# Performance work log

Hardware: AMD Instinct MI355X
Metric: run time of the kernel (lower is better)

Reference implementation:

```python
import jax, jax.numpy as jnp
import numpy as np

COMMITMENT_COST = 0.25
NUM_EMBEDDINGS = 512
EMBEDDING_DIM = 64


def setup_inputs() -> dict:
    key = jax.random.key(0)
    k1, k2 = jax.random.split(key)
    B, T = 64, 1024
    inputs = jax.random.normal(k1, (B, T, EMBEDDING_DIM), dtype=jnp.float32)
    # matches nn.Embedding init uniform_(-1/K, 1/K)
    embedding = jax.random.uniform(
        k2, (NUM_EMBEDDINGS, EMBEDDING_DIM), dtype=jnp.float32,
        minval=-1.0 / NUM_EMBEDDINGS, maxval=1.0 / NUM_EMBEDDINGS)
    return {"inputs": inputs, "embedding": embedding}


def reference(inputs, embedding):
    B = inputs.shape[0]
    K, D = embedding.shape
    flat = inputs.reshape(-1, D)  # [N, D]
    # squared-euclidean distances [N, K] (same expansion as torch source)
    distances = (
        jnp.sum(flat * flat, axis=1, keepdims=True)
        + jnp.sum(embedding * embedding, axis=1)
        - 2.0 * flat @ embedding.T
    )
    idx = jnp.argmin(distances, axis=1)  # [N]
    # one-hot @ embedding  ==  gather
    quantized = embedding[idx].reshape(inputs.shape)

    e_latent_loss = jnp.mean((jax.lax.stop_gradient(quantized) - inputs) ** 2)
    q_latent_loss = jnp.mean((quantized - jax.lax.stop_gradient(inputs)) ** 2)
    loss = q_latent_loss + COMMITMENT_COST * e_latent_loss

    # straight-through estimator
    quantized_st = inputs + jax.lax.stop_gradient(quantized - inputs)

    # avg_probs = mean of one-hot encodings == histogram of indices / N
    counts = jax.ops.segment_sum(
        jnp.ones(flat.shape[0], dtype=jnp.float32), idx, num_segments=K)
    avg_probs = counts / flat.shape[0]
    perplexity = jnp.exp(-jnp.sum(avg_probs * jnp.log(avg_probs + 1e-10)))

    indices_for_transformer = idx.reshape(B, -1)
    return loss, quantized_st, perplexity, indices_for_transformer
```

## Files before the change

### kernel.cpp

```cpp
#include <hip/hip_runtime.h>
#include <math.h>

#define D 64
#define K 512
#define BLOCK 256
#define ROWS 128
#define KT 128
#define NKT (K / KT)
#define NPART 32


__device__ __forceinline__ float np_sumsq64(const float* v) {
#pragma clang fp contract(off)
    float r[8];
#pragma unroll
    for (int m = 0; m < 8; ++m) r[m] = v[m] * v[m];
#pragma unroll
    for (int i = 8; i < 64; i += 8) {
#pragma unroll
        for (int m = 0; m < 8; ++m) r[m] = r[m] + v[i + m] * v[i + m];
    }
    return ((r[0] + r[1]) + (r[2] + r[3])) + ((r[4] + r[5]) + (r[6] + r[7]));
}

__global__ __launch_bounds__(BLOCK, 2) void vq_fused(
    const float* __restrict__ x, const float* __restrict__ emb,
    float* __restrict__ q_out, float* __restrict__ idx_out,
    float* __restrict__ block_sums, int* __restrict__ part_hist, int N)
{
    __shared__ float4 xs4[ROWS * 16];
    __shared__ float4 es4[KT * 16];
    __shared__ float sx_s[ROWS];
    __shared__ float se_s[KT];
    __shared__ int hist[K];
    __shared__ float red[BLOCK / 64];

    const int tid = threadIdx.x;
    const int rg = tid & 15;
    const int cg = tid >> 4;
    const int rowbase = blockIdx.x * ROWS;

    for (int k2 = tid; k2 < K; k2 += BLOCK) hist[k2] = 0;

    const float4* xsrc = (const float4*)(x + (size_t)rowbase * D);
#pragma unroll
    for (int i = 0; i < (ROWS * 16) / BLOCK; ++i) {
        int f = tid + i * BLOCK;
        int row = f >> 4, jc = f & 15;
        xs4[row * 16 + (jc ^ ((row >> 3) & 7))] = xsrc[f];
    }
    __syncthreads();

    if (tid < ROWS) {
        float xr[D];
        const int sw = (tid >> 3) & 7;
#pragma unroll
        for (int jc = 0; jc < 16; ++jc) {
            float4 v = xs4[tid * 16 + (jc ^ sw)];
            xr[4 * jc + 0] = v.x; xr[4 * jc + 1] = v.y;
            xr[4 * jc + 2] = v.z; xr[4 * jc + 3] = v.w;
        }
        sx_s[tid] = np_sumsq64(xr);
    }

    float bd[8], bkf[8];
#pragma unroll
    for (int r = 0; r < 8; ++r) { bd[r] = INFINITY; bkf[r] = 0.f; }

    const int xbase = rg * 8, ebase = cg * 8;
    const int swx0 = rg & 7, swe0 = cg & 7;

    for (int kt = 0; kt < NKT; ++kt) {
        const float4* esrc = (const float4*)(emb + (size_t)kt * KT * D);
#pragma unroll
        for (int i = 0; i < (KT * 16) / BLOCK; ++i) {
            int f = tid + i * BLOCK;
            int row = f >> 4, jc = f & 15;
            es4[row * 16 + (jc ^ ((row >> 3) & 7))] = esrc[f];
        }
        __syncthreads();

        if (tid < KT) {
            float er[D];
            const int sw = (tid >> 3) & 7;
#pragma unroll
            for (int jc = 0; jc < 16; ++jc) {
                float4 v = es4[tid * 16 + (jc ^ sw)];
                er[4 * jc + 0] = v.x; er[4 * jc + 1] = v.y;
                er[4 * jc + 2] = v.z; er[4 * jc + 3] = v.w;
            }
            se_s[tid] = np_sumsq64(er);
        }

        float acc[8][8];
#pragma unroll
        for (int r = 0; r < 8; ++r)
#pragma unroll
            for (int c = 0; c < 8; ++c) acc[r][c] = 0.f;

#pragma unroll 2
        for (int jc = 0; jc < 16; ++jc) {
            float4 xa[8], eb[8];
#pragma unroll
            for (int r = 0; r < 8; ++r)
                xa[r] = xs4[(xbase + r) * 16 + (jc ^ swx0)];
#pragma unroll
            for (int c = 0; c < 8; ++c)
                eb[c] = es4[(ebase + c) * 16 + (jc ^ swe0)];
#pragma unroll
            for (int r = 0; r < 8; ++r)
#pragma unroll
                for (int c = 0; c < 8; ++c) {
                    acc[r][c] = fmaf(xa[r].x, eb[c].x, acc[r][c]);
                    acc[r][c] = fmaf(xa[r].y, eb[c].y, acc[r][c]);
                    acc[r][c] = fmaf(xa[r].z, eb[c].z, acc[r][c]);
                    acc[r][c] = fmaf(xa[r].w, eb[c].w, acc[r][c]);
                }
        }
        __syncthreads();

        const int kglob = kt * KT + ebase;
        float sev[8];
#pragma unroll
        for (int c = 0; c < 8; ++c) sev[c] = se_s[ebase + c];
#pragma unroll
        for (int r = 0; r < 8; ++r) {
            float sxv = sx_s[xbase + r];
#pragma unroll
            for (int c = 0; c < 8; ++c) {
                float dcur = (sxv + sev[c]) - 2.0f * acc[r][c];
                if (dcur < bd[r]) { bd[r] = dcur; bkf[r] = (float)(kglob + c); }
            }
        }
    }

    __syncthreads();
    float2* bests = (float2*)es4;
#pragma unroll
    for (int r = 0; r < 8; ++r)
        bests[(xbase + r) * 16 + cg] = make_float2(bd[r], bkf[r]);
    __syncthreads();

    float s = 0.f;
    if (tid < ROWS) {
        float bdd = INFINITY, bjf = 1e30f;
#pragma unroll
        for (int g = 0; g < 16; ++g) {
            float2 p = bests[tid * 16 + g];
            if (p.x < bdd || (p.x == bdd && p.y < bjf)) { bdd = p.x; bjf = p.y; }
        }
        const int bi = (int)bjf;
        atomicAdd(&hist[bi], 1);

        const int rowg = rowbase + tid;
        const float4* ep = (const float4*)(emb + (size_t)bi * D);
        float4* qp = (float4*)(q_out + (size_t)rowg * D);
        const int sw = (tid >> 3) & 7;
#pragma unroll
        for (int jc = 0; jc < 16; ++jc) {
            float4 xv = xs4[tid * 16 + (jc ^ sw)];
            float4 e  = ep[jc];
            float dx0 = e.x - xv.x, dx1 = e.y - xv.y;
            float dx2 = e.z - xv.z, dx3 = e.w - xv.w;
            s = fmaf(dx0, dx0, s);
            s = fmaf(dx1, dx1, s);
            s = fmaf(dx2, dx2, s);
            s = fmaf(dx3, dx3, s);
            float4 qs;
            qs.x = xv.x + dx0; qs.y = xv.y + dx1;
            qs.z = xv.z + dx2; qs.w = xv.w + dx3;
            qp[jc] = qs;
        }
        idx_out[rowg] = (float)bi;
    }

    for (int off = 32; off; off >>= 1) s += __shfl_down(s, off, 64);
    if ((tid & 63) == 0) red[tid >> 6] = s;
    __syncthreads();
    if (tid == 0) {
        float t = 0.f;
#pragma unroll
        for (int w = 0; w < BLOCK / 64; ++w) t += red[w];
        block_sums[blockIdx.x] = t;
    }
    const int part = (int)(blockIdx.x & (NPART - 1));
    for (int k2 = tid; k2 < K; k2 += BLOCK) {
        int h = hist[k2];
        if (h) atomicAdd(&part_hist[part * K + k2], h);
    }
}

__global__ __launch_bounds__(512) void vq_finalize(
    const float* __restrict__ block_sums, int nblocks,
    const int* __restrict__ part_hist, float* __restrict__ out_loss,
    float* __restrict__ out_perp, float inv_nelem, float inv_rows)
{
    const int tid = threadIdx.x;
    double ls = 0.0;
    for (int i = tid; i < nblocks; i += 512) ls += (double)block_sums[i];
    int c = 0;
#pragma unroll
    for (int pp = 0; pp < NPART; ++pp) c += part_hist[pp * K + tid];
    double ps = 0.0;
    {
        float p = (float)c * inv_rows;
        ps = (double)(p * logf(p + 1e-10f));
    }
    for (int off = 32; off; off >>= 1) {
        ls += __shfl_down(ls, off, 64);
        ps += __shfl_down(ps, off, 64);
    }
    __shared__ double l8[8], p8[8];
    if ((tid & 63) == 0) { l8[tid >> 6] = ls; p8[tid >> 6] = ps; }
    __syncthreads();
    if (tid == 0) {
        double L = 0.0, P = 0.0;
#pragma unroll
        for (int w = 0; w < 8; ++w) { L += l8[w]; P += p8[w]; }
        *out_loss = 1.25f * (float)(L * (double)inv_nelem);
        *out_perp = expf((float)(-P));
    }
}

extern "C" void kernel_launch(void* const* d_in, const int* in_sizes, int n_in,
                              void* d_out, int out_size, void* d_ws, size_t ws_size,
                              hipStream_t stream) {
    const float* x   = (const float*)d_in[0];
    const float* emb = (const float*)d_in[1];
    const int N = in_sizes[0] / D;
    const int nblocks = N / ROWS;

    float* out      = (float*)d_out;
    float* loss_out = out;
    float* q_out    = out + 1;
    float* perp_out = out + 1 + (size_t)N * D;
    float* idx_out  = perp_out + 1;

    float* block_sums = (float*)d_ws;
    int*   part_hist  = (int*)((char*)d_ws + (((size_t)nblocks * 4 + 255) & ~(size_t)255));

    hipMemsetAsync(part_hist, 0, NPART * K * sizeof(int), stream);
    vq_fused<<<nblocks, BLOCK, 0, stream>>>(x, emb, q_out, idx_out,
                                            block_sums, part_hist, N);
    vq_finalize<<<1, 512, 0, stream>>>(block_sums, nblocks, part_hist,
                                       loss_out, perp_out,
                                       1.0f / (float)((size_t)N * D),
                                       1.0f / (float)N);
}
```

Before: 139.8 us.

## Fuse finalize into main kernel via last-block counter; precompute norms with shuffles

```diff
diff --git a/kernel.cpp b/kernel.cpp
--- a/kernel.cpp
+++ b/kernel.cpp
@@ -10,37 +10,28 @@
 #define NPART 32
 
 
-__device__ __forceinline__ float np_sumsq64(const float* v) {
-#pragma clang fp contract(off)
-    float r[8];
-#pragma unroll
-    for (int m = 0; m < 8; ++m) r[m] = v[m] * v[m];
-#pragma unroll
-    for (int i = 8; i < 64; i += 8) {
-#pragma unroll
-        for (int m = 0; m < 8; ++m) r[m] = r[m] + v[i + m] * v[i + m];
-    }
-    return ((r[0] + r[1]) + (r[2] + r[3])) + ((r[4] + r[5]) + (r[6] + r[7]));
-}
-
 __global__ __launch_bounds__(BLOCK, 2) void vq_fused(
     const float* __restrict__ x, const float* __restrict__ emb,
     float* __restrict__ q_out, float* __restrict__ idx_out,
-    float* __restrict__ block_sums, int* __restrict__ part_hist, int N)
+    float* __restrict__ block_sums, int* __restrict__ part_hist,
+    int* __restrict__ done_ctr,
+    float* __restrict__ out_loss, float* __restrict__ out_perp,
+    float inv_nelem, float inv_rows)
 {
     __shared__ float4 xs4[ROWS * 16];
     __shared__ float4 es4[KT * 16];
     __shared__ float sx_s[ROWS];
-    __shared__ float se_s[KT];
-    __shared__ int hist[K];
-    __shared__ float red[BLOCK / 64];
+    __shared__ float se_s[K];
+    __shared__ float redf[BLOCK / 64];
+    __shared__ double l8[BLOCK / 64], p8[BLOCK / 64];
+    __shared__ int flag_s;
 
     const int tid = threadIdx.x;
+    const int lane = tid & 63;
+    const int wv = tid >> 6;
     const int rg = tid & 15;
     const int cg = tid >> 4;
     const int rowbase = blockIdx.x * ROWS;
-
-    for (int k2 = tid; k2 < K; k2 += BLOCK) hist[k2] = 0;
 
     const float4* xsrc = (const float4*)(x + (size_t)rowbase * D);
 #pragma unroll
@@ -49,19 +40,47 @@
         int row = f >> 4, jc = f & 15;
         xs4[row * 16 + (jc ^ ((row >> 3) & 7))] = xsrc[f];
     }
-    __syncthreads();
-
-    if (tid < ROWS) {
-        float xr[D];
-        const int sw = (tid >> 3) & 7;
-#pragma unroll
-        for (int jc = 0; jc < 16; ++jc) {
-            float4 v = xs4[tid * 16 + (jc ^ sw)];
-            xr[4 * jc + 0] = v.x; xr[4 * jc + 1] = v.y;
-            xr[4 * jc + 2] = v.z; xr[4 * jc + 3] = v.w;
-        }
-        sx_s[tid] = np_sumsq64(xr);
-    }
+
+    {
+#pragma clang fp contract(off)
+#pragma unroll
+        for (int rnd = 0; rnd < (ROWS * 8) / BLOCK; ++rnd) {
+            int slot = tid + rnd * BLOCK;
+            int r = slot >> 3, m = slot & 7;
+            const float* xp = x + (size_t)(rowbase + r) * D + m;
+            float v = xp[0];
+            float rm = v * v;
+#pragma unroll
+            for (int t = 1; t < 8; ++t) {
+                v = xp[8 * t];
+                rm = rm + v * v;
+            }
+            float o;
+            o = __shfl_xor(rm, 1, 64); rm = rm + o;
+            o = __shfl_xor(rm, 2, 64); rm = rm + o;
+            o = __shfl_xor(rm, 4, 64); rm = rm + o;
+            if (m == 0) sx_s[r] = rm;
+        }
+#pragma unroll
+        for (int rnd = 0; rnd < (K * 8) / BLOCK; ++rnd) {
+            int slot = tid + rnd * BLOCK;
+            int r = slot >> 3, m = slot & 7;
+            const float* ep = emb + (size_t)r * D + m;
+            float v = ep[0];
+            float rm = v * v;
+#pragma unroll
+            for (int t = 1; t < 8; ++t) {
+                v = ep[8 * t];
+                rm = rm + v * v;
+            }
+            float o;
+            o = __shfl_xor(rm, 1, 64); rm = rm + o;
+            o = __shfl_xor(rm, 2, 64); rm = rm + o;
+            o = __shfl_xor(rm, 4, 64); rm = rm + o;
+            if (m == 0) se_s[r] = rm;
+        }
+    }
+    __syncthreads();
 
     float bd[8], bkf[8];
 #pragma unroll
@@ -70,6 +89,7 @@
     const int xbase = rg * 8, ebase = cg * 8;
     const int swx0 = rg & 7, swe0 = cg & 7;
 
+#pragma unroll 1
     for (int kt = 0; kt < NKT; ++kt) {
         const float4* esrc = (const float4*)(emb + (size_t)kt * KT * D);
 #pragma unroll
@@ -79,18 +99,6 @@
             es4[row * 16 + (jc ^ ((row >> 3) & 7))] = esrc[f];
         }
         __syncthreads();
-
-        if (tid < KT) {
-            float er[D];
-            const int sw = (tid >> 3) & 7;
-#pragma unroll
-            for (int jc = 0; jc < 16; ++jc) {
-                float4 v = es4[tid * 16 + (jc ^ sw)];
-                er[4 * jc + 0] = v.x; er[4 * jc + 1] = v.y;
-                er[4 * jc + 2] = v.z; er[4 * jc + 3] = v.w;
-            }
-            se_s[tid] = np_sumsq64(er);
-        }
 
         float acc[8][8];
 #pragma unroll
@@ -122,7 +130,7 @@
         const int kglob = kt * KT + ebase;
         float sev[8];
 #pragma unroll
-        for (int c = 0; c < 8; ++c) sev[c] = se_s[ebase + c];
+        for (int c = 0; c < 8; ++c) sev[c] = se_s[kglob + c];
 #pragma unroll
         for (int r = 0; r < 8; ++r) {
             float sxv = sx_s[xbase + r];
@@ -134,7 +142,6 @@
         }
     }
 
-    __syncthreads();
     float2* bests = (float2*)es4;
 #pragma unroll
     for (int r = 0; r < 8; ++r)
@@ -150,7 +157,7 @@
             if (p.x < bdd || (p.x == bdd && p.y < bjf)) { bdd = p.x; bjf = p.y; }
         }
         const int bi = (int)bjf;
-        atomicAdd(&hist[bi], 1);
+        atomicAdd(&part_hist[(blockIdx.x & (NPART - 1)) * K + bi], 1);
 
         const int rowg = rowbase + tid;
         const float4* ep = (const float4*)(emb + (size_t)bi * D);
@@ -175,48 +182,47 @@
     }
 
     for (int off = 32; off; off >>= 1) s += __shfl_down(s, off, 64);
-    if ((tid & 63) == 0) red[tid >> 6] = s;
+    if (lane == 0) redf[wv] = s;
     __syncthreads();
     if (tid == 0) {
         float t = 0.f;
 #pragma unroll
-        for (int w = 0; w < BLOCK / 64; ++w) t += red[w];
+        for (int w = 0; w < BLOCK / 64; ++w) t += redf[w];
         block_sums[blockIdx.x] = t;
     }
-    const int part = (int)(blockIdx.x & (NPART - 1));
+
+    __threadfence();
+    __syncthreads();
+    if (tid == 0) flag_s = atomicAdd(done_ctr, 1);
+    __syncthreads();
+    if (flag_s != (int)gridDim.x - 1) return;
+
+    __threadfence();
+    const int nblocks = (int)gridDim.x;
+    double ls = 0.0;
+    for (int i = tid; i < nblocks; i += BLOCK)
+        ls += (double)__hip_atomic_load(&block_sums[i], __ATOMIC_RELAXED,
+                                        __HIP_MEMORY_SCOPE_AGENT);
+    double ps = 0.0;
     for (int k2 = tid; k2 < K; k2 += BLOCK) {
-        int h = hist[k2];
-        if (h) atomicAdd(&part_hist[part * K + k2], h);
-    }
-}
-
-__global__ __launch_bounds__(512) void vq_finalize(
-    const float* __restrict__ block_sums, int nblocks,
-    const int* __restrict__ part_hist, float* __restrict__ out_loss,
-    float* __restrict__ out_perp, float inv_nelem, float inv_rows)
-{
-    const int tid = threadIdx.x;
-    double ls = 0.0;
-    for (int i = tid; i < nblocks; i += 512) ls += (double)block_sums[i];
-    int c = 0;
-#pragma unroll
-    for (int pp = 0; pp < NPART; ++pp) c += part_hist[pp * K + tid];
-    double ps = 0.0;
-    {
-        float p = (float)c * inv_rows;
-        ps = (double)(p * logf(p + 1e-10f));
+        int c = 0;
+#pragma unroll
+        for (int p = 0; p < NPART; ++p)
+            c += __hip_atomic_load(&part_hist[p * K + k2], __ATOMIC_RELAXED,
+                                   __HIP_MEMORY_SCOPE_AGENT);
+        float pv = (float)c * inv_rows;
+        ps += (double)(pv * logf(pv + 1e-10f));
     }
     for (int off = 32; off; off >>= 1) {
         ls += __shfl_down(ls, off, 64);
         ps += __shfl_down(ps, off, 64);
     }
-    __shared__ double l8[8], p8[8];
-    if ((tid & 63) == 0) { l8[tid >> 6] = ls; p8[tid >> 6] = ps; }
+    if (lane == 0) { l8[wv] = ls; p8[wv] = ps; }
     __syncthreads();
     if (tid == 0) {
         double L = 0.0, P = 0.0;
 #pragma unroll
-        for (int w = 0; w < 8; ++w) { L += l8[w]; P += p8[w]; }
+        for (int w = 0; w < BLOCK / 64; ++w) { L += l8[w]; P += p8[w]; }
         *out_loss = 1.25f * (float)(L * (double)inv_nelem);
         *out_perp = expf((float)(-P));
     }
@@ -237,13 +243,15 @@
     float* idx_out  = perp_out + 1;
 
     float* block_sums = (float*)d_ws;
-    int*   part_hist  = (int*)((char*)d_ws + (((size_t)nblocks * 4 + 255) & ~(size_t)255));
-
-    hipMemsetAsync(part_hist, 0, NPART * K * sizeof(int), stream);
+    int*   part_hist  = (int*)((char*)d_ws +
+                               (((size_t)nblocks * 4 + 255) & ~(size_t)255));
+    int*   done_ctr   = part_hist + (size_t)NPART * K;
+
+    hipMemsetAsync(part_hist, 0, (size_t)NPART * K * sizeof(int) + sizeof(int),
+                   stream);
     vq_fused<<<nblocks, BLOCK, 0, stream>>>(x, emb, q_out, idx_out,
-                                            block_sums, part_hist, N);
-    vq_finalize<<<1, 512, 0, stream>>>(block_sums, nblocks, part_hist,
-                                       loss_out, perp_out,
-                                       1.0f / (float)((size_t)N * D),
-                                       1.0f / (float)N);
+                                            block_sums, part_hist, done_ctr,
+                                            loss_out, perp_out,
+                                            1.0f / (float)((size_t)N * D),
+                                            1.0f / (float)N);
 }
```

Measured after the change: 201.4 us. 44.1% more time.
